# Kernel tuning notes

Measured on AMD Instinct MI355X. Metric: run time of the kernel, lower is better.

Reference implementation:

```python
import jax, jax.numpy as jnp
import numpy as np

M, K, N = 4096, 4096, 11008


def setup_inputs() -> dict:
    key = jax.random.key(0)
    k1, k2, k3 = jax.random.split(key, 3)
    x = jax.random.normal(k1, (M, K), dtype=jnp.float16)
    weight_packed = jax.random.randint(k2, ((K + 1) // 2, N), 0, 256, dtype=jnp.int32)
    weight_scale = jax.random.uniform(k3, (N,), dtype=jnp.float32) * 0.05 + 1e-3
    return {"x": x, "weight_packed": weight_packed, "weight_scale": weight_scale}


def reference(x, weight_packed, weight_scale):
    # Unpack int4 nibbles: low nibble -> even K index, high nibble -> odd K index.
    packed = weight_packed.astype(jnp.uint8)                      # [K//2, N]
    low = (packed & 15).astype(jnp.float32) - 8.0                 # even rows
    high = ((packed >> 4) & 15).astype(jnp.float32) - 8.0         # odd rows
    k = x.shape[-1]
    w = jnp.stack([low, high], axis=1).reshape(-1, low.shape[1])[:k]  # [K, N]
    # Per-output-feature symmetric scale, then fp16 GEMM (matches torch fallback).
    w = (w * weight_scale[None, :]).astype(jnp.float16)
    out = jnp.matmul(x, w)                                        # [M, N] fp16
    return out
```

## Files before the change

### kernel.cpp

```cpp
#include <hip/hip_runtime.h>
#include <hip/hip_fp16.h>
#include <stdint.h>


#define M_DIM 4096
#define K_DIM 4096
#define N_DIM 11008
#define KH    (K_DIM / 2)

#define WS_XH_BYTES  ((size_t)M_DIM * K_DIM * 2)

typedef __attribute__((ext_vector_type(8))) _Float16 f16x8;
typedef __attribute__((ext_vector_type(2))) _Float16 h2;
typedef __attribute__((ext_vector_type(4))) float f32x4;

__device__ __forceinline__ unsigned pack_f16_pair(float lo, float hi) {
    return __builtin_bit_cast(unsigned, __builtin_amdgcn_cvt_pkrtz(lo, hi));
}

__device__ __forceinline__ unsigned dq_pair(unsigned v) {
    unsigned c = (v & 0xFu) | ((v << 12) & 0x000F0000u) | 0x64006400u;
    h2 r = __builtin_bit_cast(h2, c) + __builtin_bit_cast(h2, 0xE408E408u);
    return __builtin_bit_cast(unsigned, r);
}

__device__ __forceinline__ void gld_lds16(const void* g, void* l) {
    __builtin_amdgcn_global_load_lds(
        (const __attribute__((address_space(1))) unsigned int*)g,
        (__attribute__((address_space(3))) unsigned int*)l,
        16, 0, 0);
}

__global__ void __launch_bounds__(256) cvt_x_kernel(
    const float* __restrict__ X, unsigned short* __restrict__ Xh)
{
    size_t i = ((size_t)blockIdx.x * 256 + threadIdx.x) * 8;
    float4 a = *(const float4*)(X + i);
    float4 b = *(const float4*)(X + i + 4);
    uint4 o = make_uint4(pack_f16_pair(a.x, a.y), pack_f16_pair(a.z, a.w),
                         pack_f16_pair(b.x, b.y), pack_f16_pair(b.z, b.w));
    *(uint4*)(Xh + i) = o;
}

__global__ void __launch_bounds__(256) dqt_kernel(
    const int* __restrict__ WP, unsigned* __restrict__ Wt)
{
    __shared__ unsigned Lt[64][65];
    const int t = threadIdx.x;
    const int n0 = blockIdx.x * 64;
    const int r0 = blockIdx.y * 64;
    const int g = t >> 6, l = t & 63;
#pragma unroll
    for (int i = 0; i < 16; ++i) {
        const int r = r0 + g * 16 + i;
        Lt[l][g * 16 + i] = dq_pair((unsigned)WP[(size_t)r * N_DIM + n0 + l]);
    }
    __syncthreads();
    const int nr = t >> 2, sg = t & 3;
    unsigned* dst = Wt + (size_t)(n0 + nr) * KH + r0 + sg * 16;
#pragma unroll
    for (int c = 0; c < 4; ++c) {
        uint4 v = make_uint4(Lt[nr][sg * 16 + c * 4 + 0], Lt[nr][sg * 16 + c * 4 + 1],
                             Lt[nr][sg * 16 + c * 4 + 2], Lt[nr][sg * 16 + c * 4 + 3]);
        *(uint4*)(dst + c * 4) = v;
    }
}

__global__ void __launch_bounds__(512, 2) qgemm7_kernel(
    const unsigned short* __restrict__ Xh,
    const unsigned*       __restrict__ Wt,
    const float*          __restrict__ WS,
    float*                __restrict__ Out)
{
    __shared__ unsigned short LA[2][2][8192];
    __shared__ unsigned short LB[2][2][8192];

    const int t = threadIdx.x;
    const int w = t >> 6;
    const int l = t & 63;

    const int bid = blockIdx.x;
    const int xcd = bid & 7;
    const int i8  = bid >> 3;
    const int bx  = i8 >> 1;
    const int by  = (xcd << 1) | (i8 & 1);
    const int bm0 = by * 256;
    const int bn0 = bx * 256;

    const int wr = w >> 2;
    const int wc = w & 3;

    f32x4 acc[8][4];
#pragma unroll
    for (int i = 0; i < 8; ++i)
#pragma unroll
        for (int j = 0; j < 4; ++j)
            acc[i][j] = (f32x4){0.f, 0.f, 0.f, 0.f};

    const int cS = (t & 7) ^ ((t >> 3) & 7);
    const unsigned short* gA0 = Xh + (size_t)(bm0 + (t >> 3)) * K_DIM + cS * 8;
    const unsigned*       gB0 = Wt + (size_t)(bn0 + (t >> 3)) * KH + cS * 4;
    const int t8 = t * 8;

#define SB_H(buf, h, kt) do {                                                 \
    gld_lds16(gB0 + (size_t)((h) * 128) * KH + (size_t)(kt) * 32,             \
              &LB[buf][h][t8]);                                               \
    gld_lds16(gB0 + (size_t)((h) * 128 + 64) * KH + (size_t)(kt) * 32,        \
              &LB[buf][h][4096 + t8]);                                        \
} while (0)

#define SA_C0(buf, kt) do {                                                   \
    gld_lds16(gA0 + (size_t)(kt) * 64,                  &LA[buf][0][t8]);     \
    gld_lds16(gA0 + (size_t)128 * K_DIM + (size_t)(kt) * 64, &LA[buf][1][t8]); \
} while (0)

#define SA_C1(buf, kt) do {                                                   \
    gld_lds16(gA0 + (size_t)64 * K_DIM + (size_t)(kt) * 64,                   \
              &LA[buf][0][4096 + t8]);                                        \
    gld_lds16(gA0 + (size_t)192 * K_DIM + (size_t)(kt) * 64,                  \
              &LA[buf][1][4096 + t8]);                                        \
} while (0)

    const int lq = l >> 4;
    const int lr = l & 15;

    f16x8 af0[4][2], af1[4][2], bf0[2][2], bf1[2][2];

#define READ_AF(D, MH, ARR) do {                                              \
    _Pragma("unroll")                                                         \
    for (int mi = 0; mi < 4; ++mi) {                                          \
        const int row = (MH) * 64 + mi * 16 + lr;                             \
        _Pragma("unroll")                                                     \
        for (int ks = 0; ks < 2; ++ks)                                        \
            ARR[mi][ks] = *(const f16x8*)                                     \
                &LA[D][wr][row * 64 + (((ks * 4 + lq) ^ (row & 7)) * 8)];     \
    }                                                                         \
} while (0)

#define READ_BF(D, NH, ARR) do {                                              \
    _Pragma("unroll")                                                         \
    for (int n = 0; n < 2; ++n) {                                             \
        const int row = (wc & 1) * 64 + ((NH) * 2 + n) * 16 + lr;             \
        _Pragma("unroll")                                                     \
        for (int ks = 0; ks < 2; ++ks)                                        \
            ARR[n][ks] = *(const f16x8*)                                      \
                &LB[D][wc >> 1][row * 64 + (((ks * 4 + lq) ^ (row & 7)) * 8)]; \
    }                                                                         \
} while (0)

#define MFMA_Q(MH, NH, AFA, BFA) do {                                         \
    __builtin_amdgcn_s_setprio(1);                                            \
    _Pragma("unroll")                                                         \
    for (int mi = 0; mi < 4; ++mi)                                            \
        _Pragma("unroll")                                                     \
        for (int n = 0; n < 2; ++n)                                           \
            _Pragma("unroll")                                                 \
            for (int ks = 0; ks < 2; ++ks)                                    \
                acc[(MH) * 4 + mi][(NH) * 2 + n] =                            \
                    __builtin_amdgcn_mfma_f32_16x16x32_f16(                   \
                        AFA[mi][ks], BFA[n][ks],                              \
                        acc[(MH) * 4 + mi][(NH) * 2 + n], 0, 0, 0);           \
    __builtin_amdgcn_s_setprio(0);                                            \
} while (0)

#define WAITV(n) asm volatile("s_waitcnt vmcnt(" #n ")" ::: "memory")
#define LGKM0()  do { asm volatile("s_waitcnt lgkmcnt(0)" ::: "memory");      \
                      __builtin_amdgcn_sched_barrier(0); } while (0)
#define BAR()    __builtin_amdgcn_s_barrier()

#define TILE_FULL(D, KTN) do {                                                \
    WAITV(2); BAR();                         \
    READ_AF(D, 0, af0); READ_BF(D, 0, bf0); READ_BF(D, 1, bf1);               \
    SB_H(D ^ 1, 0, KTN); BAR(); LGKM0();                                      \
    MFMA_Q(0, 0, af0, bf0); BAR();                                            \
    SB_H(D ^ 1, 1, KTN); BAR();                                               \
    MFMA_Q(0, 1, af0, bf1); BAR();                                            \
    WAITV(4); BAR();                             \
    SA_C0(D ^ 1, KTN); READ_AF(D, 1, af1); BAR(); LGKM0();                    \
    MFMA_Q(1, 1, af1, bf1); BAR();                                            \
    SA_C1(D ^ 1, KTN); BAR();                                                 \
    MFMA_Q(1, 0, af1, bf0); BAR();                                            \
} while (0)

#define TILE_LAST(D) do {                                                     \
    WAITV(2); BAR();                                                          \
    READ_AF(D, 0, af0); READ_BF(D, 0, bf0); READ_BF(D, 1, bf1);               \
    BAR(); LGKM0();                                                           \
    MFMA_Q(0, 0, af0, bf0); BAR();                                            \
    MFMA_Q(0, 1, af0, bf1); BAR();                                            \
    WAITV(0); BAR();                                                          \
    READ_AF(D, 1, af1); BAR(); LGKM0();                                       \
    MFMA_Q(1, 1, af1, bf1); BAR();                                            \
    MFMA_Q(1, 0, af1, bf0);                                                   \
} while (0)

    SB_H(0, 0, 0); SB_H(0, 1, 0); SA_C0(0, 0); SA_C1(0, 0);

    for (int i = 0; i < 31; ++i) {
        TILE_FULL(0, 2 * i + 1);
        TILE_FULL(1, 2 * i + 2);
    }
    TILE_FULL(0, 63);
    TILE_LAST(1);

#pragma unroll
    for (int ni = 0; ni < 4; ++ni) {
        const int col = bn0 + wc * 64 + ni * 16 + lr;
        const float s = WS[col];
#pragma unroll
        for (int mi = 0; mi < 8; ++mi) {
            const int row = bm0 + wr * 128 + mi * 16 + lq * 4;
#pragma unroll
            for (int i = 0; i < 4; ++i) {
                Out[(size_t)(row + i) * N_DIM + col] = acc[mi][ni][i] * s;
            }
        }
    }
#undef SB_H
#undef SA_C0
#undef SA_C1
#undef READ_AF
#undef READ_BF
#undef MFMA_Q
#undef WAITV
#undef LGKM0
#undef BAR
#undef TILE_FULL
#undef TILE_LAST
}

extern "C" void kernel_launch(void* const* d_in, const int* in_sizes, int n_in,
                              void* d_out, int out_size, void* d_ws, size_t ws_size,
                              hipStream_t stream) {
    const float* X  = (const float*)d_in[0];
    const int*   WP = (const int*)d_in[1];
    const float* WS = (const float*)d_in[2];
    float*       Out = (float*)d_out;

    unsigned short* Xh = (unsigned short*)d_ws;
    unsigned*       Wt = (unsigned*)((char*)d_ws + WS_XH_BYTES);

    cvt_x_kernel<<<(M_DIM * K_DIM) / (256 * 8), 256, 0, stream>>>(X, Xh);
    dim3 gdq(N_DIM / 64, KH / 64);
    dqt_kernel<<<gdq, 256, 0, stream>>>(WP, Wt);
    dim3 grid((N_DIM / 256) * (M_DIM / 256));
    qgemm7_kernel<<<grid, 512, 0, stream>>>(Xh, Wt, WS, Out);
}
```

Baseline: 474.4 us.

## Rework GEMM main-loop schedule with fewer barriers and interleaved global-to-LDS loads

Replaces the per-tile pipeline, which had about ten workgroup barriers, with a schedule that has two barriers per K tile. Weight and activation global-to-LDS copies for the next buffer are spread between the four MFMA quadrants, and wait counts are adjusted to match. The MFMA loop order now puts the K sub-step outermost. The goal is less barrier stall time and better overlap of loads with matrix math. The cost is that correctness now depends on careful buffer-reuse ordering across waves.

```diff
diff --git a/kernel.cpp b/kernel.cpp
--- a/kernel.cpp
+++ b/kernel.cpp
@@ -66,7 +66,7 @@
     }
 }
 
-__global__ void __launch_bounds__(512, 2) qgemm7_kernel(
+__global__ void __launch_bounds__(512, 2) qgemm9_kernel(
     const unsigned short* __restrict__ Xh,
     const unsigned*       __restrict__ Wt,
     const float*          __restrict__ WS,
@@ -98,68 +98,56 @@
             acc[i][j] = (f32x4){0.f, 0.f, 0.f, 0.f};
 
     const int cS = (t & 7) ^ ((t >> 3) & 7);
-    const unsigned short* gA0 = Xh + (size_t)(bm0 + (t >> 3)) * K_DIM + cS * 8;
-    const unsigned*       gB0 = Wt + (size_t)(bn0 + (t >> 3)) * KH + cS * 4;
+    const unsigned short* gA = Xh + (size_t)(bm0 + (t >> 3)) * K_DIM + cS * 8;
+    const unsigned*       gB = Wt + (size_t)(bn0 + (t >> 3)) * KH + cS * 4;
     const int t8 = t * 8;
 
-#define SB_H(buf, h, kt) do {                                                 \
-    gld_lds16(gB0 + (size_t)((h) * 128) * KH + (size_t)(kt) * 32,             \
-              &LB[buf][h][t8]);                                               \
-    gld_lds16(gB0 + (size_t)((h) * 128 + 64) * KH + (size_t)(kt) * 32,        \
-              &LB[buf][h][4096 + t8]);                                        \
-} while (0)
-
-#define SA_C0(buf, kt) do {                                                   \
-    gld_lds16(gA0 + (size_t)(kt) * 64,                  &LA[buf][0][t8]);     \
-    gld_lds16(gA0 + (size_t)128 * K_DIM + (size_t)(kt) * 64, &LA[buf][1][t8]); \
-} while (0)
-
-#define SA_C1(buf, kt) do {                                                   \
-    gld_lds16(gA0 + (size_t)64 * K_DIM + (size_t)(kt) * 64,                   \
-              &LA[buf][0][4096 + t8]);                                        \
-    gld_lds16(gA0 + (size_t)192 * K_DIM + (size_t)(kt) * 64,                  \
-              &LA[buf][1][4096 + t8]);                                        \
-} while (0)
+#define SU_A(buf, h, c, kt)                                                   \
+    gld_lds16(gA + (size_t)((h) * 128 + (c) * 64) * K_DIM + (size_t)(kt) * 64, \
+              &LA[buf][h][(c) * 4096 + t8])
+#define SU_B(buf, bh, ch, kt)                                                 \
+    gld_lds16(gB + (size_t)((bh) * 128 + (ch) * 64) * KH + (size_t)(kt) * 32, \
+              &LB[buf][bh][(ch) * 4096 + t8])
 
     const int lq = l >> 4;
     const int lr = l & 15;
 
     f16x8 af0[4][2], af1[4][2], bf0[2][2], bf1[2][2];
 
-#define READ_AF(D, MH, ARR) do {                                              \
+#define READ_AF(D, h, ARR) do {                                               \
     _Pragma("unroll")                                                         \
     for (int mi = 0; mi < 4; ++mi) {                                          \
-        const int row = (MH) * 64 + mi * 16 + lr;                             \
+        const int lrow = (h) * 64 + mi * 16 + lr;                             \
         _Pragma("unroll")                                                     \
         for (int ks = 0; ks < 2; ++ks)                                        \
             ARR[mi][ks] = *(const f16x8*)                                     \
-                &LA[D][wr][row * 64 + (((ks * 4 + lq) ^ (row & 7)) * 8)];     \
+                &LA[D][wr][lrow * 64 + (((ks * 4 + lq) ^ (lrow & 7)) * 8)];   \
     }                                                                         \
 } while (0)
 
-#define READ_BF(D, NH, ARR) do {                                              \
+#define READ_BF(D, ch, ARR) do {                                              \
     _Pragma("unroll")                                                         \
     for (int n = 0; n < 2; ++n) {                                             \
-        const int row = (wc & 1) * 64 + ((NH) * 2 + n) * 16 + lr;             \
+        const int lrow = (wc & 1) * 64 + (ch) * 32 + n * 16 + lr;             \
         _Pragma("unroll")                                                     \
         for (int ks = 0; ks < 2; ++ks)                                        \
             ARR[n][ks] = *(const f16x8*)                                      \
-                &LB[D][wc >> 1][row * 64 + (((ks * 4 + lq) ^ (row & 7)) * 8)]; \
+                &LB[D][wc >> 1][lrow * 64 + (((ks * 4 + lq) ^ (lrow & 7)) * 8)]; \
     }                                                                         \
 } while (0)
 
-#define MFMA_Q(MH, NH, AFA, BFA) do {                                         \
+#define Q16(MB, AF, BF, NB) do {                                              \
     __builtin_amdgcn_s_setprio(1);                                            \
     _Pragma("unroll")                                                         \
-    for (int mi = 0; mi < 4; ++mi)                                            \
+    for (int ks = 0; ks < 2; ++ks)                                            \
         _Pragma("unroll")                                                     \
-        for (int n = 0; n < 2; ++n)                                           \
+        for (int mi = 0; mi < 4; ++mi)                                        \
             _Pragma("unroll")                                                 \
-            for (int ks = 0; ks < 2; ++ks)                                    \
-                acc[(MH) * 4 + mi][(NH) * 2 + n] =                            \
+            for (int n = 0; n < 2; ++n)                                       \
+                acc[(MB) + mi][(NB) + n] =                                    \
                     __builtin_amdgcn_mfma_f32_16x16x32_f16(                   \
-                        AFA[mi][ks], BFA[n][ks],                              \
-                        acc[(MH) * 4 + mi][(NH) * 2 + n], 0, 0, 0);           \
+                        AF[mi][ks], BF[n][ks], acc[(MB) + mi][(NB) + n],      \
+                        0, 0, 0);                                             \
     __builtin_amdgcn_s_setprio(0);                                            \
 } while (0)
 
@@ -168,39 +156,42 @@
                       __builtin_amdgcn_sched_barrier(0); } while (0)
 #define BAR()    __builtin_amdgcn_s_barrier()
 
-#define TILE_FULL(D, KTN) do {                                                \
-    WAITV(2); BAR();                         \
-    READ_AF(D, 0, af0); READ_BF(D, 0, bf0); READ_BF(D, 1, bf1);               \
-    SB_H(D ^ 1, 0, KTN); BAR(); LGKM0();                                      \
-    MFMA_Q(0, 0, af0, bf0); BAR();                                            \
-    SB_H(D ^ 1, 1, KTN); BAR();                                               \
-    MFMA_Q(0, 1, af0, bf1); BAR();                                            \
-    WAITV(4); BAR();                             \
-    SA_C0(D ^ 1, KTN); READ_AF(D, 1, af1); BAR(); LGKM0();                    \
-    MFMA_Q(1, 1, af1, bf1); BAR();                                            \
-    SA_C1(D ^ 1, KTN); BAR();                                                 \
-    MFMA_Q(1, 0, af1, bf0); BAR();                                            \
+#define TILE_STD(D, DN, ktn) do {                                             \
+    SU_B(DN, 0, 0, ktn); SU_B(DN, 0, 1, ktn);                                 \
+    WAITV(4); BAR();                                                          \
+    READ_AF(D, 0, af0); READ_BF(D, 0, bf0); LGKM0();                          \
+    Q16(0, af0, bf0, 0);                                                      \
+    SU_B(DN, 1, 0, ktn); SU_B(DN, 1, 1, ktn);                                 \
+    READ_BF(D, 1, bf1); LGKM0();                                              \
+    Q16(0, af0, bf1, 2);                                                      \
+    SU_A(DN, 0, 0, ktn); SU_A(DN, 1, 0, ktn);                                 \
+    WAITV(6); BAR();                                                          \
+    READ_AF(D, 1, af1); LGKM0();                                              \
+    Q16(4, af1, bf1, 2);                                                      \
+    SU_A(DN, 0, 1, ktn); SU_A(DN, 1, 1, ktn);                                 \
+    Q16(4, af1, bf0, 0);                                                      \
 } while (0)
 
 #define TILE_LAST(D) do {                                                     \
     WAITV(2); BAR();                                                          \
-    READ_AF(D, 0, af0); READ_BF(D, 0, bf0); READ_BF(D, 1, bf1);               \
-    BAR(); LGKM0();                                                           \
-    MFMA_Q(0, 0, af0, bf0); BAR();                                            \
-    MFMA_Q(0, 1, af0, bf1); BAR();                                            \
+    READ_AF(D, 0, af0); READ_BF(D, 0, bf0); LGKM0();                          \
+    Q16(0, af0, bf0, 0);                                                      \
+    READ_BF(D, 1, bf1); LGKM0();                                              \
+    Q16(0, af0, bf1, 2);                                                      \
     WAITV(0); BAR();                                                          \
-    READ_AF(D, 1, af1); BAR(); LGKM0();                                       \
-    MFMA_Q(1, 1, af1, bf1); BAR();                                            \
-    MFMA_Q(1, 0, af1, bf0);                                                   \
-} while (0)
-
-    SB_H(0, 0, 0); SB_H(0, 1, 0); SA_C0(0, 0); SA_C1(0, 0);
+    READ_AF(D, 1, af1); LGKM0();                                              \
+    Q16(4, af1, bf1, 2);                                                      \
+    Q16(4, af1, bf0, 0);                                                      \
+} while (0)
+
+    SU_B(0, 0, 0, 0); SU_B(0, 0, 1, 0); SU_B(0, 1, 0, 0); SU_B(0, 1, 1, 0);
+    SU_A(0, 0, 0, 0); SU_A(0, 1, 0, 0); SU_A(0, 0, 1, 0); SU_A(0, 1, 1, 0);
 
     for (int i = 0; i < 31; ++i) {
-        TILE_FULL(0, 2 * i + 1);
-        TILE_FULL(1, 2 * i + 2);
-    }
-    TILE_FULL(0, 63);
+        TILE_STD(0, 1, 2 * i + 1);
+        TILE_STD(1, 0, 2 * i + 2);
+    }
+    TILE_STD(0, 1, 63);
     TILE_LAST(1);
 
 #pragma unroll
@@ -216,16 +207,15 @@
             }
         }
     }
-#undef SB_H
-#undef SA_C0
-#undef SA_C1
+#undef SU_A
+#undef SU_B
 #undef READ_AF
 #undef READ_BF
-#undef MFMA_Q
+#undef Q16
 #undef WAITV
 #undef LGKM0
 #undef BAR
-#undef TILE_FULL
+#undef TILE_STD
 #undef TILE_LAST
 }
 
@@ -244,5 +234,5 @@
     dim3 gdq(N_DIM / 64, KH / 64);
     dqt_kernel<<<gdq, 256, 0, stream>>>(WP, Wt);
     dim3 grid((N_DIM / 256) * (M_DIM / 256));
-    qgemm7_kernel<<<grid, 512, 0, stream>>>(Xh, Wt, WS, Out);
-}
+    qgemm9_kernel<<<grid, 512, 0, stream>>>(Xh, Wt, WS, Out);
+}
```

Result: faster. 408.8 us, median of 2 (-13.8%).
